# Optimization experiments

Measured on AMD Instinct MI355X. Metric: run time of the kernel, lower is better.

## Reference

```python
import jax, jax.numpy as jnp
import numpy as np

WH, WW = 8, 8
NUM_HEADS = 8
DIM = 256
MLP_HIDDEN = 1024
EPS = 1e-5


def _rel_pos_index(wh, ww):
    ch, cw = np.meshgrid(np.arange(wh), np.arange(ww), indexing='ij')
    flat = np.stack([ch.ravel(), cw.ravel()])            # (2, N)
    rel = flat[:, :, None] - flat[:, None, :]            # (2, N, N)
    rel = rel.transpose(1, 2, 0).copy()                  # (N, N, 2)
    rel[:, :, 0] += wh - 1
    rel[:, :, 1] += ww - 1
    rel[:, :, 0] *= 2 * ww - 1
    return jnp.asarray(rel.sum(-1))                      # (N, N) int

REL_IDX = _rel_pos_index(WH, WW)


def _layernorm(x, g, b):
    mu = x.mean(-1, keepdims=True)
    var = ((x - mu) ** 2).mean(-1, keepdims=True)
    return (x - mu) * jax.lax.rsqrt(var + EPS) * g + b


def _window_partition(x):
    B, H, W, C = x.shape
    x = x.reshape(B, H // WH, WH, W // WW, WW, C)
    return x.transpose(0, 1, 3, 2, 4, 5).reshape(-1, WH * WW, C)


def _window_reverse(w, B, H, W):
    C = w.shape[-1]
    x = w.reshape(B, H // WH, W // WW, WH, WW, C)
    return x.transpose(0, 1, 3, 2, 4, 5).reshape(B, H, W, C)


def _window_attn(qx, kvx, qw, qb, kvw, kvb, bias_table, pw, pb):
    # qx/kvx: [Bw, N, C]; weights stored as [in, out] (torch Linear transposed)
    Bw, N, C = qx.shape
    hd = C // NUM_HEADS
    scale = hd ** -0.5
    q = (qx @ qw + qb).reshape(Bw, N, NUM_HEADS, hd).transpose(0, 2, 1, 3) * scale
    kv = (kvx @ kvw + kvb).reshape(Bw, N, 2, NUM_HEADS, hd)
    k = kv[:, :, 0].transpose(0, 2, 1, 3)
    v = kv[:, :, 1].transpose(0, 2, 1, 3)
    attn = jnp.einsum('bhnd,bhmd->bhnm', q, k)
    bias = bias_table[REL_IDX.reshape(-1)].reshape(N, N, NUM_HEADS).transpose(2, 0, 1)
    attn = jax.nn.softmax(attn + bias[None], axis=-1)
    out = jnp.einsum('bhnm,bhmd->bhnd', attn, v).transpose(0, 2, 1, 3).reshape(Bw, N, C)
    return out @ pw + pb


def setup_inputs() -> dict:
    key = jax.random.key(0)
    ks = jax.random.split(key, 16)
    B, H, W, C = 4, 160, 160, DIM
    nW = (H // WH) * (W // WW)
    N = WH * WW
    n_bias = (2 * WH - 1) * (2 * WW - 1)  # 225
    s = 0.02
    return {
        'x': jax.random.normal(ks[0], (B, H, W, C), jnp.float32),
        'enc_feat': jax.random.normal(ks[1], (B, H, W, C), jnp.float32),
        'mask_matrix': jnp.zeros((nW, N, N), jnp.float32),
        'norm1_g': jnp.ones((C,), jnp.float32),
        'norm1_b': jnp.zeros((C,), jnp.float32),
        'q1_w': jax.random.normal(ks[2], (C, C), jnp.float32) * s,
        'q1_b': jnp.zeros((C,), jnp.float32),
        'kv1_w': jax.random.normal(ks[3], (C, 2 * C), jnp.float32) * s,
        'kv1_b': jnp.zeros((2 * C,), jnp.float32),
        'bias1': jax.random.normal(ks[4], (n_bias, NUM_HEADS), jnp.float32) * s,
        'proj1_w': jax.random.normal(ks[5], (C, C), jnp.float32) * s,
        'proj1_b': jnp.zeros((C,), jnp.float32),
        'q2_w': jax.random.normal(ks[6], (C, C), jnp.float32) * s,
        'q2_b': jnp.zeros((C,), jnp.float32),
        'kv2_w': jax.random.normal(ks[7], (C, 2 * C), jnp.float32) * s,
        'kv2_b': jnp.zeros((2 * C,), jnp.float32),
        'bias2': jax.random.normal(ks[8], (n_bias, NUM_HEADS), jnp.float32) * s,
        'proj2_w': jax.random.normal(ks[9], (C, C), jnp.float32) * s,
        'proj2_b': jnp.zeros((C,), jnp.float32),
        'norm2_g': jnp.ones((C,), jnp.float32),
        'norm2_b': jnp.zeros((C,), jnp.float32),
        'fc1_w': jax.random.normal(ks[10], (C, MLP_HIDDEN), jnp.float32) * s,
        'fc1_b': jnp.zeros((MLP_HIDDEN,), jnp.float32),
        'fc2_w': jax.random.normal(ks[11], (MLP_HIDDEN, C), jnp.float32) * s,
        'fc2_b': jnp.zeros((C,), jnp.float32),
    }


def reference(x, enc_feat, mask_matrix, norm1_g, norm1_b, q1_w, q1_b, kv1_w, kv1_b,
              bias1, proj1_w, proj1_b, q2_w, q2_b, kv2_w, kv2_b, bias2, proj2_w,
              proj2_b, norm2_g, norm2_b, fc1_w, fc1_b, fc2_w, fc2_b):
    # NOTE: the source forward never passes mask_matrix into attention; faithful here.
    B, H, W, C = x.shape
    shortcut = x
    xn = _layernorm(x, norm1_g, norm1_b)
    xw = _window_partition(xn)              # [B*nW, N, C]
    ew = _window_partition(enc_feat)        # [B*nW, N, C]
    # windowed self-attention with relative position bias
    xw = _window_attn(xw, xw, q1_w, q1_b, kv1_w, kv1_b, bias1, proj1_w, proj1_b)
    # windowed cross-attention to encoder features
    xw = _window_attn(xw, ew, q2_w, q2_b, kv2_w, kv2_b, bias2, proj2_w, proj2_b)
    x = shortcut + _window_reverse(xw, B, H, W)
    h = _layernorm(x, norm2_g, norm2_b)
    h = jax.nn.gelu(h @ fc1_w + fc1_b, approximate=False) @ fc2_w + fc2_b
    return x + h
```

## Files before the change

### kernel.cpp

```cpp
#include <hip/hip_runtime.h>

typedef __attribute__((ext_vector_type(4))) float f32x4;
typedef __attribute__((ext_vector_type(8))) short bf16x8;
typedef __attribute__((ext_vector_type(8))) unsigned short ushort8;
typedef unsigned short u16;
typedef unsigned int u32;

#define LDS_AS(p) ((__attribute__((address_space(3))) void*)(p))
#define GLB_AS(p) ((const __attribute__((address_space(1))) void*)(p))

__device__ __forceinline__ u16 f2b(float f) {
    u32 u = __builtin_bit_cast(u32, f);
    u32 r = (u + 0x7fffu + ((u >> 16) & 1u)) >> 16;
    return (u16)r;
}

struct PrepAll {
    const float* src[8];
    u16* dst[8];
    int K[8];
    int N[8];
    float S[8];
};

__global__ __launch_bounds__(256) void prep_w(PrepAll p) {
    const int wi = blockIdx.y;
    const int K = p.K[wi], N = p.N[wi];
    const int e = blockIdx.x * 256 + threadIdx.x;
    if (e >= K * N) return;
    const int k = e / N, n = e % N;
    p.dst[wi][n * K + k] = f2b(p.src[wi][e] * p.S[wi]);
}

__global__ __launch_bounds__(64) void prep_bias(const float* __restrict__ t1,
                                                const float* __restrict__ t2,
                                                float* __restrict__ Bm) {
    const int j = threadIdx.x;
    const int i = blockIdx.x;
    const int hh = blockIdx.y;
    const int s = hh >> 3, h = hh & 7;
    const int idx = ((i >> 3) - (j >> 3) + 7) * 15 + ((i & 7) - (j & 7) + 7);
    const float* tab = s ? t2 : t1;
    Bm[(long)hh * 4096 + i * 64 + j] = tab[idx * 8 + h];
}

__global__ __launch_bounds__(256) void prep_bcat(const float* __restrict__ q1b,
                                                 const float* __restrict__ kv1b,
                                                 const float* __restrict__ q2b,
                                                 float qs, float* __restrict__ b1cat,
                                                 float* __restrict__ q2bs) {
    const int g = blockIdx.x * 256 + threadIdx.x;
    if (g < 256) {
        b1cat[g] = qs * q1b[g];
        q2bs[g] = qs * q2b[g];
    } else if (g < 768) {
        b1cat[g] = kv1b[g - 256];
    }
}

__global__ __launch_bounds__(256) void cast_bf(const float* __restrict__ in,
                                               u16* __restrict__ out) {
    const long i = (long)blockIdx.x * 256 + threadIdx.x;
    const float4 a = *(const float4*)(in + i * 8);
    const float4 b = *(const float4*)(in + i * 8 + 4);
    ushort8 o;
    o[0] = f2b(a.x); o[1] = f2b(a.y); o[2] = f2b(a.z); o[3] = f2b(a.w);
    o[4] = f2b(b.x); o[5] = f2b(b.y); o[6] = f2b(b.z); o[7] = f2b(b.w);
    *(ushort8*)(out + i * 8) = o;
}

__global__ __launch_bounds__(256) void ln256(const float* __restrict__ x,
                                             const float* __restrict__ g,
                                             const float* __restrict__ b,
                                             u16* __restrict__ out) {
    const int lane = threadIdx.x & 63;
    const long row = (long)blockIdx.x * 4 + (threadIdx.x >> 6);
    const float4 v = *(const float4*)(x + row * 256 + lane * 4);
    float s = v.x + v.y + v.z + v.w;
    float s2 = v.x * v.x + v.y * v.y + v.z * v.z + v.w * v.w;
#pragma unroll
    for (int off = 32; off > 0; off >>= 1) {
        s += __shfl_xor(s, off);
        s2 += __shfl_xor(s2, off);
    }
    const float mu = s * (1.f / 256.f);
    const float var = s2 * (1.f / 256.f) - mu * mu;
    const float rr = rsqrtf(var + 1e-5f);
    const int c = lane * 4;
    const float4 gv = *(const float4*)(g + c);
    const float4 bv = *(const float4*)(b + c);
    ushort4 o;
    o.x = f2b((v.x - mu) * rr * gv.x + bv.x);
    o.y = f2b((v.y - mu) * rr * gv.y + bv.y);
    o.z = f2b((v.z - mu) * rr * gv.z + bv.z);
    o.w = f2b((v.w - mu) * rr * gv.w + bv.w);
    *(ushort4*)(out + row * 256 + c) = o;
}

template <int EPI>
__global__ __launch_bounds__(256) void gemm128(const u16* __restrict__ A,
                                               const u16* __restrict__ Bt,
                                               const float* __restrict__ bias,
                                               const float* __restrict__ res,
                                               u16* outb, float* outf,
                                               int N, int K, int Nt) {
    __shared__ u16 lds[2][2][128 * 32];
    const int t = threadIdx.x;
    const int lane = t & 63;
    const int wave = t >> 6;
    const int wr = wave >> 1, wc = wave & 1;
    const int l15 = lane & 15, lg = lane >> 4;

    const int per = gridDim.x >> 3;
    const int id2 = (blockIdx.x & 7) * per + (blockIdx.x >> 3);
    const int bm = id2 / Nt, bn = id2 % Nt;
    const long m0 = (long)bm * 128;
    const int n0 = bn * 128;

    const u16* Ag = A + (m0 + (t >> 2)) * K + (t & 3) * 8;
    const u16* Bg = Bt + (long)(n0 + (t >> 2)) * K + (t & 3) * 8;

    const int nt = K >> 5;

    auto stage = [&](int b, int k0) {
        u16* Al = lds[b][0] + t * 8;
        u16* Bl = lds[b][1] + t * 8;
        __builtin_amdgcn_global_load_lds(GLB_AS(Ag + k0), LDS_AS(Al), 16, 0, 0);
        __builtin_amdgcn_global_load_lds(GLB_AS(Ag + (long)64 * K + k0), LDS_AS(Al + 2048), 16, 0, 0);
        __builtin_amdgcn_global_load_lds(GLB_AS(Bg + k0), LDS_AS(Bl), 16, 0, 0);
        __builtin_amdgcn_global_load_lds(GLB_AS(Bg + (long)64 * K + k0), LDS_AS(Bl + 2048), 16, 0, 0);
    };

    f32x4 acc[4][4];
#pragma unroll
    for (int i = 0; i < 4; i++)
#pragma unroll
        for (int j = 0; j < 4; j++) acc[i][j] = (f32x4){0.f, 0.f, 0.f, 0.f};

    stage(0, 0);
    if (nt > 1) stage(1, 32);

    for (int tt = 0; tt < nt; ++tt) {
        const int cur = tt & 1;
        if (tt < nt - 1)
            asm volatile("s_waitcnt vmcnt(4)" ::: "memory");
        else
            asm volatile("s_waitcnt vmcnt(0)" ::: "memory");
        __builtin_amdgcn_s_barrier();

        bf16x8 af[4], bfr[4];
#pragma unroll
        for (int i = 0; i < 4; i++)
            af[i] = *(const bf16x8*)(lds[cur][0] + (wr * 64 + i * 16 + l15) * 32 + lg * 8);
#pragma unroll
        for (int i = 0; i < 4; i++)
            bfr[i] = *(const bf16x8*)(lds[cur][1] + (wc * 64 + i * 16 + l15) * 32 + lg * 8);
        asm volatile("s_waitcnt lgkmcnt(0)" ::: "memory");
        __builtin_amdgcn_sched_barrier(0);
        __builtin_amdgcn_s_barrier();

        if (tt + 2 < nt) stage(cur, (tt + 2) * 32);

#pragma unroll
        for (int mi = 0; mi < 4; mi++)
#pragma unroll
            for (int ni = 0; ni < 4; ni++)
                acc[mi][ni] = __builtin_amdgcn_mfma_f32_16x16x32_bf16(af[mi], bfr[ni], acc[mi][ni], 0, 0, 0);
    }

#pragma unroll
    for (int mi = 0; mi < 4; mi++) {
#pragma unroll
        for (int ni = 0; ni < 4; ni++) {
            const int col = n0 + wc * 64 + ni * 16 + l15;
            const float bv = bias[col];
#pragma unroll
            for (int r = 0; r < 4; r++) {
                const long row = m0 + wr * 64 + mi * 16 + lg * 4 + r;
                float v = acc[mi][ni][r] + bv;
                if (EPI == 2) v = 0.5f * v * (1.f + erff(v * 0.70710678118f));
                const long idx = row * N + col;
                if (EPI == 3)
                    outf[idx] = v + res[idx];
                else
                    outb[idx] = f2b(v);
            }
        }
    }
}

__global__ __launch_bounds__(256) void attn64(const u16* __restrict__ Q, int qs,
                                              const u16* __restrict__ KV, int ks,
                                              const float* __restrict__ Bm,
                                              u16* __restrict__ AO) {
    __shared__ u16 Plds[4][64 * 72];
    __shared__ u16 Vt[4][32 * 72];
    const int lane = threadIdx.x & 63, wave = threadIdx.x >> 6;
    const int wh = blockIdx.x * 4 + wave;
    const int w = wh >> 3, h = wh & 7;
    const int b = w / 400, rem = w % 400;
    const int wy = rem / 20, wx = rem % 20;
    const long base_t = (long)b * 25600 + wy * 8 * 160 + wx * 8;
    const int l15 = lane & 15, lg = lane >> 4;

    bf16x8 qf[4], kf[4];
#pragma unroll
    for (int ti = 0; ti < 4; ti++) {
        const int r = ti * 16 + l15;
        const long tt = base_t + (r >> 3) * 160 + (r & 7);
        qf[ti] = *(const bf16x8*)(Q + tt * qs + h * 32 + lg * 8);
        kf[ti] = *(const bf16x8*)(KV + tt * ks + h * 32 + lg * 8);
    }
    const f32x4 zz = (f32x4){0.f, 0.f, 0.f, 0.f};
    f32x4 s[4][4];
#pragma unroll
    for (int ti = 0; ti < 4; ti++)
#pragma unroll
        for (int tj = 0; tj < 4; tj++)
            s[ti][tj] = __builtin_amdgcn_mfma_f32_16x16x32_bf16(qf[ti], kf[tj], zz, 0, 0, 0);

    {
        const long tt = base_t + (lane >> 3) * 160 + (lane & 7);
        const u16* vrow = KV + tt * ks + 256 + h * 32;
#pragma unroll
        for (int cg = 0; cg < 4; cg++) {
            bf16x8 v8 = *(const bf16x8*)(vrow + cg * 8);
#pragma unroll
            for (int j = 0; j < 8; j++) Vt[wave][(cg * 8 + j) * 72 + lane] = (u16)v8[j];
        }
    }

    const float* Bh = Bm + h * 4096;
#pragma unroll
    for (int ti = 0; ti < 4; ti++) {
#pragma unroll
        for (int r = 0; r < 4; r++) {
            const int i = ti * 16 + lg * 4 + r;
            float vv[4];
            float m = -1e30f;
#pragma unroll
            for (int tj = 0; tj < 4; tj++) {
                vv[tj] = s[ti][tj][r] + Bh[i * 64 + tj * 16 + l15];
                m = fmaxf(m, vv[tj]);
            }
#pragma unroll
            for (int off = 1; off < 16; off <<= 1) m = fmaxf(m, __shfl_xor(m, off));
            float sum = 0.f;
#pragma unroll
            for (int tj = 0; tj < 4; tj++) {
                vv[tj] = __expf(vv[tj] - m);
                sum += vv[tj];
            }
#pragma unroll
            for (int off = 1; off < 16; off <<= 1) sum += __shfl_xor(sum, off);
            const float inv = 1.f / sum;
#pragma unroll
            for (int tj = 0; tj < 4; tj++)
                Plds[wave][i * 72 + tj * 16 + l15] = f2b(vv[tj] * inv);
        }
    }

    f32x4 o[4][2];
#pragma unroll
    for (int mi = 0; mi < 4; mi++)
#pragma unroll
        for (int n = 0; n < 2; n++) o[mi][n] = zz;
#pragma unroll
    for (int c = 0; c < 2; c++) {
        bf16x8 vf[2];
#pragma unroll
        for (int n = 0; n < 2; n++)
            vf[n] = *(const bf16x8*)(&Vt[wave][(n * 16 + l15) * 72 + c * 32 + lg * 8]);
#pragma unroll
        for (int mi = 0; mi < 4; mi++) {
            bf16x8 pf = *(const bf16x8*)(&Plds[wave][(mi * 16 + l15) * 72 + c * 32 + lg * 8]);
#pragma unroll
            for (int n = 0; n < 2; n++)
                o[mi][n] = __builtin_amdgcn_mfma_f32_16x16x32_bf16(pf, vf[n], o[mi][n], 0, 0, 0);
        }
    }
#pragma unroll
    for (int mi = 0; mi < 4; mi++) {
#pragma unroll
        for (int n = 0; n < 2; n++) {
#pragma unroll
            for (int r = 0; r < 4; r++) {
                const int i = mi * 16 + lg * 4 + r;
                const long tt = base_t + (i >> 3) * 160 + (i & 7);
                AO[tt * 256 + h * 32 + n * 16 + l15] = f2b(o[mi][n][r]);
            }
        }
    }
}

extern "C" void kernel_launch(void* const* d_in, const int* in_sizes, int n_in,
                              void* d_out, int out_size, void* d_ws, size_t ws_size,
                              hipStream_t stream) {
    const float* x    = (const float*)d_in[0];
    const float* enc  = (const float*)d_in[1];
    const float* n1g  = (const float*)d_in[3];
    const float* n1b  = (const float*)d_in[4];
    const float* q1w  = (const float*)d_in[5];
    const float* q1b  = (const float*)d_in[6];
    const float* kv1w = (const float*)d_in[7];
    const float* kv1b = (const float*)d_in[8];
    const float* bias1 = (const float*)d_in[9];
    const float* p1w  = (const float*)d_in[10];
    const float* p1b  = (const float*)d_in[11];
    const float* q2w  = (const float*)d_in[12];
    const float* q2b  = (const float*)d_in[13];
    const float* kv2w = (const float*)d_in[14];
    const float* kv2b = (const float*)d_in[15];
    const float* bias2 = (const float*)d_in[16];
    const float* p2w  = (const float*)d_in[17];
    const float* p2b  = (const float*)d_in[18];
    const float* n2g  = (const float*)d_in[19];
    const float* n2b  = (const float*)d_in[20];
    const float* f1w  = (const float*)d_in[21];
    const float* f1b  = (const float*)d_in[22];
    const float* f2w  = (const float*)d_in[23];
    const float* f2bias = (const float*)d_in[24];
    float* out = (float*)d_out;

    char* ws = (char*)d_ws;
    size_t off = 0;
    auto alloc = [&](size_t bytes) {
        char* p = ws + off;
        off += (bytes + 255) & ~(size_t)255;
        return p;
    };
    u16* Wt    = (u16*)alloc(1048576 * 2);
    float* Bm  = (float*)alloc(16 * 4096 * 4);
    float* b1c = (float*)alloc(768 * 4);
    float* q2s = (float*)alloc(256 * 4);
    u16* xn    = (u16*)alloc(52428800);
    u16* qb    = (u16*)alloc(52428800);
    u16* kvb   = (u16*)alloc(104857600);
    u16* ao    = (u16*)alloc(52428800);
    u16* encb  = (u16*)alloc(52428800);

    u16* qkv = qb;
    u16* h1  = kvb;

    u16 *q1t = Wt, *p1t = Wt + 196608, *q2t = Wt + 262144,
        *kv2t = Wt + 327680, *p2t = Wt + 458752, *f1t = Wt + 524288, *f2t = Wt + 786432;

    const float qscale = 0.17677669529663687f;

    PrepAll pa;
    pa.src[0] = q1w;  pa.dst[0] = q1t;          pa.K[0] = 256;  pa.N[0] = 256;  pa.S[0] = qscale;
    pa.src[1] = kv1w; pa.dst[1] = Wt + 65536;   pa.K[1] = 256;  pa.N[1] = 512;  pa.S[1] = 1.f;
    pa.src[2] = p1w;  pa.dst[2] = p1t;          pa.K[2] = 256;  pa.N[2] = 256;  pa.S[2] = 1.f;
    pa.src[3] = q2w;  pa.dst[3] = q2t;          pa.K[3] = 256;  pa.N[3] = 256;  pa.S[3] = qscale;
    pa.src[4] = kv2w; pa.dst[4] = kv2t;         pa.K[4] = 256;  pa.N[4] = 512;  pa.S[4] = 1.f;
    pa.src[5] = p2w;  pa.dst[5] = p2t;          pa.K[5] = 256;  pa.N[5] = 256;  pa.S[5] = 1.f;
    pa.src[6] = f1w;  pa.dst[6] = f1t;          pa.K[6] = 256;  pa.N[6] = 1024; pa.S[6] = 1.f;
    pa.src[7] = f2w;  pa.dst[7] = f2t;          pa.K[7] = 1024; pa.N[7] = 256;  pa.S[7] = 1.f;
    prep_w<<<dim3(1024, 8), 256, 0, stream>>>(pa);
    prep_bias<<<dim3(64, 16), 64, 0, stream>>>(bias1, bias2, Bm);
    prep_bcat<<<dim3(3), 256, 0, stream>>>(q1b, kv1b, q2b, qscale, b1c, q2s);
    cast_bf<<<dim3(12800), 256, 0, stream>>>(enc, encb);
    ln256<<<dim3(25600), 256, 0, stream>>>(x, n1g, n1b, xn);

    gemm128<0><<<dim3(4800), 256, 0, stream>>>(xn, q1t, b1c, nullptr, qkv, nullptr, 768, 256, 6);
    attn64<<<dim3(3200), 256, 0, stream>>>(qkv, 768, qkv + 256, 768, Bm, ao);
    gemm128<0><<<dim3(1600), 256, 0, stream>>>(ao, p1t, p1b, nullptr, xn, nullptr, 256, 256, 2);

    gemm128<0><<<dim3(1600), 256, 0, stream>>>(xn, q2t, q2s, nullptr, qb, nullptr, 256, 256, 2);
    gemm128<0><<<dim3(3200), 256, 0, stream>>>(encb, kv2t, kv2b, nullptr, kvb, nullptr, 512, 256, 4);
    attn64<<<dim3(3200), 256, 0, stream>>>(qb, 256, kvb, 512, Bm + 8 * 4096, ao);

    gemm128<3><<<dim3(1600), 256, 0, stream>>>(ao, p2t, p2b, x, (u16*)nullptr, out, 256, 256, 2);

    ln256<<<dim3(25600), 256, 0, stream>>>(out, n2g, n2b, qb);
    for (int c = 0; c < 2; c++) {
        const u16* xh = qb + (size_t)c * 51200 * 256;
        float* oc = out + (size_t)c * 51200 * 256;
        gemm128<2><<<dim3(3200), 256, 0, stream>>>(xh, f1t, f1b, nullptr, h1, nullptr, 1024, 256, 8);
        gemm128<3><<<dim3(800), 256, 0, stream>>>(h1, f2t, f2bias, oc, (u16*)nullptr, oc, 256, 1024, 2);
    }
}
```

Baseline: 800.9 us.

## Replace direct global-to-LDS GEMM staging with register-prefetched padded LDS pipeline

The GEMM kernel no longer uses global_load_lds. It now prefetches tiles into registers three stages ahead, writes them into a padded LDS layout (row stride 40) to avoid bank conflicts, and uses one barrier per k-step instead of two. K is now a template parameter so the loop fully unrolls, and launch bounds request 3 blocks per CU. The trade is more register use and VGPR-to-LDS write traffic in exchange for fewer bank conflicts, fewer barriers and deeper latency hiding.

```diff
diff --git a/kernel.cpp b/kernel.cpp
--- a/kernel.cpp
+++ b/kernel.cpp
@@ -5,9 +5,6 @@
 typedef __attribute__((ext_vector_type(8))) unsigned short ushort8;
 typedef unsigned short u16;
 typedef unsigned int u32;
-
-#define LDS_AS(p) ((__attribute__((address_space(3))) void*)(p))
-#define GLB_AS(p) ((const __attribute__((address_space(1))) void*)(p))
 
 __device__ __forceinline__ u16 f2b(float f) {
     u32 u = __builtin_bit_cast(u32, f);
@@ -97,14 +94,18 @@
     *(ushort4*)(out + row * 256 + c) = o;
 }
 
-template <int EPI>
-__global__ __launch_bounds__(256) void gemm128(const u16* __restrict__ A,
-                                               const u16* __restrict__ Bt,
-                                               const float* __restrict__ bias,
-                                               const float* __restrict__ res,
-                                               u16* outb, float* outf,
-                                               int N, int K, int Nt) {
-    __shared__ u16 lds[2][2][128 * 32];
+#define LSTR 40
+
+template <int EPI, int NT>
+__global__ __launch_bounds__(256, 3) void gemmP(const u16* __restrict__ A,
+                                                const u16* __restrict__ Bt,
+                                                const float* __restrict__ bias,
+                                                const float* __restrict__ res,
+                                                u16* outb, float* outf,
+                                                int N, int Nt) {
+    constexpr int K = NT * 32;
+    __shared__ u16 ldsA[2][128 * LSTR];
+    __shared__ u16 ldsB[2][128 * LSTR];
     const int t = threadIdx.x;
     const int lane = t & 63;
     const int wave = t >> 6;
@@ -117,19 +118,27 @@
     const long m0 = (long)bm * 128;
     const int n0 = bn * 128;
 
-    const u16* Ag = A + (m0 + (t >> 2)) * K + (t & 3) * 8;
-    const u16* Bg = Bt + (long)(n0 + (t >> 2)) * K + (t & 3) * 8;
-
-    const int nt = K >> 5;
-
-    auto stage = [&](int b, int k0) {
-        u16* Al = lds[b][0] + t * 8;
-        u16* Bl = lds[b][1] + t * 8;
-        __builtin_amdgcn_global_load_lds(GLB_AS(Ag + k0), LDS_AS(Al), 16, 0, 0);
-        __builtin_amdgcn_global_load_lds(GLB_AS(Ag + (long)64 * K + k0), LDS_AS(Al + 2048), 16, 0, 0);
-        __builtin_amdgcn_global_load_lds(GLB_AS(Bg + k0), LDS_AS(Bl), 16, 0, 0);
-        __builtin_amdgcn_global_load_lds(GLB_AS(Bg + (long)64 * K + k0), LDS_AS(Bl + 2048), 16, 0, 0);
-    };
+    const int srow = t >> 2, skc = (t & 3) * 8;
+    const u16* Ag = A + (m0 + srow) * K + skc;
+    const u16* Bg = Bt + (long)(n0 + srow) * K + skc;
+
+    bf16x8 ra[3][2], rb[3][2];
+
+#define LOAD_TILE(s, kt)                                            \
+    do {                                                            \
+        ra[s][0] = *(const bf16x8*)(Ag + (kt) * 32);                \
+        ra[s][1] = *(const bf16x8*)(Ag + (long)64 * K + (kt) * 32); \
+        rb[s][0] = *(const bf16x8*)(Bg + (kt) * 32);                \
+        rb[s][1] = *(const bf16x8*)(Bg + (long)64 * K + (kt) * 32); \
+    } while (0)
+
+#define WRITE_TILE(s, buf)                                              \
+    do {                                                                \
+        *(bf16x8*)&ldsA[buf][srow * LSTR + skc] = ra[s][0];             \
+        *(bf16x8*)&ldsA[buf][(srow + 64) * LSTR + skc] = ra[s][1];      \
+        *(bf16x8*)&ldsB[buf][srow * LSTR + skc] = rb[s][0];             \
+        *(bf16x8*)&ldsB[buf][(srow + 64) * LSTR + skc] = rb[s][1];      \
+    } while (0)
 
     f32x4 acc[4][4];
 #pragma unroll
@@ -137,36 +146,42 @@
 #pragma unroll
         for (int j = 0; j < 4; j++) acc[i][j] = (f32x4){0.f, 0.f, 0.f, 0.f};
 
-    stage(0, 0);
-    if (nt > 1) stage(1, 32);
-
-    for (int tt = 0; tt < nt; ++tt) {
+    LOAD_TILE(0, 0);
+    if (NT > 1) LOAD_TILE(1, 1);
+    if (NT > 2) LOAD_TILE(2, 2);
+    WRITE_TILE(0, 0);
+    asm volatile("s_waitcnt lgkmcnt(0)" ::: "memory");
+    __builtin_amdgcn_s_barrier();
+    __builtin_amdgcn_sched_barrier(0);
+
+#pragma unroll
+    for (int tt = 0; tt < NT; ++tt) {
         const int cur = tt & 1;
-        if (tt < nt - 1)
-            asm volatile("s_waitcnt vmcnt(4)" ::: "memory");
-        else
-            asm volatile("s_waitcnt vmcnt(0)" ::: "memory");
-        __builtin_amdgcn_s_barrier();
-
         bf16x8 af[4], bfr[4];
 #pragma unroll
         for (int i = 0; i < 4; i++)
-            af[i] = *(const bf16x8*)(lds[cur][0] + (wr * 64 + i * 16 + l15) * 32 + lg * 8);
+            af[i] = *(const bf16x8*)&ldsA[cur][(wr * 64 + i * 16 + l15) * LSTR + lg * 8];
 #pragma unroll
         for (int i = 0; i < 4; i++)
-            bfr[i] = *(const bf16x8*)(lds[cur][1] + (wc * 64 + i * 16 + l15) * 32 + lg * 8);
-        asm volatile("s_waitcnt lgkmcnt(0)" ::: "memory");
-        __builtin_amdgcn_sched_barrier(0);
-        __builtin_amdgcn_s_barrier();
-
-        if (tt + 2 < nt) stage(cur, (tt + 2) * 32);
+            bfr[i] = *(const bf16x8*)&ldsB[cur][(wc * 64 + i * 16 + l15) * LSTR + lg * 8];
+
+        if (tt + 3 < NT) LOAD_TILE(tt % 3, tt + 3);
+        if (tt + 1 < NT) WRITE_TILE((tt + 1) % 3, 1 - cur);
 
 #pragma unroll
         for (int mi = 0; mi < 4; mi++)
 #pragma unroll
             for (int ni = 0; ni < 4; ni++)
                 acc[mi][ni] = __builtin_amdgcn_mfma_f32_16x16x32_bf16(af[mi], bfr[ni], acc[mi][ni], 0, 0, 0);
-    }
+
+        if (tt + 1 < NT) {
+            asm volatile("s_waitcnt lgkmcnt(0)" ::: "memory");
+            __builtin_amdgcn_s_barrier();
+            __builtin_amdgcn_sched_barrier(0);
+        }
+    }
+#undef LOAD_TILE
+#undef WRITE_TILE
 
 #pragma unroll
     for (int mi = 0; mi < 4; mi++) {
@@ -348,35 +363,35 @@
     const float qscale = 0.17677669529663687f;
 
     PrepAll pa;
-    pa.src[0] = q1w;  pa.dst[0] = q1t;          pa.K[0] = 256;  pa.N[0] = 256;  pa.S[0] = qscale;
-    pa.src[1] = kv1w; pa.dst[1] = Wt + 65536;   pa.K[1] = 256;  pa.N[1] = 512;  pa.S[1] = 1.f;
-    pa.src[2] = p1w;  pa.dst[2] = p1t;          pa.K[2] = 256;  pa.N[2] = 256;  pa.S[2] = 1.f;
-    pa.src[3] = q2w;  pa.dst[3] = q2t;          pa.K[3] = 256;  pa.N[3] = 256;  pa.S[3] = qscale;
-    pa.src[4] = kv2w; pa.dst[4] = kv2t;         pa.K[4] = 256;  pa.N[4] = 512;  pa.S[4] = 1.f;
-    pa.src[5] = p2w;  pa.dst[5] = p2t;          pa.K[5] = 256;  pa.N[5] = 256;  pa.S[5] = 1.f;
-    pa.src[6] = f1w;  pa.dst[6] = f1t;          pa.K[6] = 256;  pa.N[6] = 1024; pa.S[6] = 1.f;
-    pa.src[7] = f2w;  pa.dst[7] = f2t;          pa.K[7] = 1024; pa.N[7] = 256;  pa.S[7] = 1.f;
+    pa.src[0] = q1w;  pa.dst[0] = q1t;        pa.K[0] = 256;  pa.N[0] = 256;  pa.S[0] = qscale;
+    pa.src[1] = kv1w; pa.dst[1] = Wt + 65536; pa.K[1] = 256;  pa.N[1] = 512;  pa.S[1] = 1.f;
+    pa.src[2] = p1w;  pa.dst[2] = p1t;        pa.K[2] = 256;  pa.N[2] = 256;  pa.S[2] = 1.f;
+    pa.src[3] = q2w;  pa.dst[3] = q2t;        pa.K[3] = 256;  pa.N[3] = 256;  pa.S[3] = qscale;
+    pa.src[4] = kv2w; pa.dst[4] = kv2t;       pa.K[4] = 256;  pa.N[4] = 512;  pa.S[4] = 1.f;
+    pa.src[5] = p2w;  pa.dst[5] = p2t;        pa.K[5] = 256;  pa.N[5] = 256;  pa.S[5] = 1.f;
+    pa.src[6] = f1w;  pa.dst[6] = f1t;        pa.K[6] = 256;  pa.N[6] = 1024; pa.S[6] = 1.f;
+    pa.src[7] = f2w;  pa.dst[7] = f2t;        pa.K[7] = 1024; pa.N[7] = 256;  pa.S[7] = 1.f;
     prep_w<<<dim3(1024, 8), 256, 0, stream>>>(pa);
     prep_bias<<<dim3(64, 16), 64, 0, stream>>>(bias1, bias2, Bm);
     prep_bcat<<<dim3(3), 256, 0, stream>>>(q1b, kv1b, q2b, qscale, b1c, q2s);
     cast_bf<<<dim3(12800), 256, 0, stream>>>(enc, encb);
     ln256<<<dim3(25600), 256, 0, stream>>>(x, n1g, n1b, xn);
 
-    gemm128<0><<<dim3(4800), 256, 0, stream>>>(xn, q1t, b1c, nullptr, qkv, nullptr, 768, 256, 6);
+    gemmP<0, 8><<<dim3(4800), 256, 0, stream>>>(xn, q1t, b1c, nullptr, qkv, nullptr, 768, 6);
     attn64<<<dim3(3200), 256, 0, stream>>>(qkv, 768, qkv + 256, 768, Bm, ao);
-    gemm128<0><<<dim3(1600), 256, 0, stream>>>(ao, p1t, p1b, nullptr, xn, nullptr, 256, 256, 2);
-
-    gemm128<0><<<dim3(1600), 256, 0, stream>>>(xn, q2t, q2s, nullptr, qb, nullptr, 256, 256, 2);
-    gemm128<0><<<dim3(3200), 256, 0, stream>>>(encb, kv2t, kv2b, nullptr, kvb, nullptr, 512, 256, 4);
+    gemmP<0, 8><<<dim3(1600), 256, 0, stream>>>(ao, p1t, p1b, nullptr, xn, nullptr, 256, 2);
+
+    gemmP<0, 8><<<dim3(1600), 256, 0, stream>>>(xn, q2t, q2s, nullptr, qb, nullptr, 256, 2);
+    gemmP<0, 8><<<dim3(3200), 256, 0, stream>>>(encb, kv2t, kv2b, nullptr, kvb, nullptr, 512, 4);
     attn64<<<dim3(3200), 256, 0, stream>>>(qb, 256, kvb, 512, Bm + 8 * 4096, ao);
 
-    gemm128<3><<<dim3(1600), 256, 0, stream>>>(ao, p2t, p2b, x, (u16*)nullptr, out, 256, 256, 2);
+    gemmP<3, 8><<<dim3(1600), 256, 0, stream>>>(ao, p2t, p2b, x, (u16*)nullptr, out, 256, 2);
 
     ln256<<<dim3(25600), 256, 0, stream>>>(out, n2g, n2b, qb);
     for (int c = 0; c < 2; c++) {
         const u16* xh = qb + (size_t)c * 51200 * 256;
         float* oc = out + (size_t)c * 51200 * 256;
-        gemm128<2><<<dim3(3200), 256, 0, stream>>>(xh, f1t, f1b, nullptr, h1, nullptr, 1024, 256, 8);
-        gemm128<3><<<dim3(800), 256, 0, stream>>>(h1, f2t, f2bias, oc, (u16*)nullptr, oc, 256, 1024, 2);
-    }
-}
+        gemmP<2, 8><<<dim3(3200), 256, 0, stream>>>(xh, f1t, f1b, nullptr, h1, nullptr, 1024, 8);
+        gemmP<3, 32><<<dim3(800), 256, 0, stream>>>(h1, f2t, f2bias, oc, (u16*)nullptr, oc, 256, 2);
+    }
+}
```

Result: no change. 794.3 us (-0.8%).
